# Kernel tuning notes

Hardware: AMD Instinct MI355X
Metric: run time of the kernel (lower is better)

The kernel has to match this reference:

```python
import jax, jax.numpy as jnp
import numpy as np

B, T = 192, 50
VOCAB = 24000
EMBED = 300
HID2 = 2000          # 2*HIDDEN_SIZE
MAXOUT = 300         # DIMEN_MAXOUT_UNIT
QV = 300             # DIMEN_QUALITY_VECTOR
H2 = 100             # LSTM hidden


def setup_inputs():
    key = jax.random.key(0)
    ks = jax.random.split(key, 24)
    s = 0.02
    inp = {
        'dec_out': jax.random.normal(ks[0], (B, T, HID2), jnp.float32),
        'y': jax.random.randint(ks[1], (B, T), 0, VOCAB, jnp.int64 if jax.config.jax_enable_x64 else jnp.int32),
        'contex': jax.random.normal(ks[2], (B, T, HID2), jnp.float32),
        'embed_table': jax.random.normal(ks[3], (VOCAB, EMBED), jnp.float32) * s,
        'W1': jax.random.uniform(ks[4], (VOCAB, QV), jnp.float32),  # torch.rand
        'S_w': jax.random.normal(ks[5], (2 * MAXOUT, HID2), jnp.float32) * s,
        'S_b': jnp.zeros((2 * MAXOUT,), jnp.float32),
        'V_w': jax.random.normal(ks[6], (2 * MAXOUT, 2 * EMBED), jnp.float32) * s,
        'V_b': jnp.zeros((2 * MAXOUT,), jnp.float32),
        'C0_w': jax.random.normal(ks[7], (2 * MAXOUT, HID2), jnp.float32) * s,
        'C0_b': jnp.zeros((2 * MAXOUT,), jnp.float32),
        'W2_w': jax.random.normal(ks[8], (QV, MAXOUT), jnp.float32) * s,
        'W2_b': jnp.zeros((QV,), jnp.float32),
        'wih0': jax.random.normal(ks[9], (4 * H2, QV), jnp.float32) * s,
        'whh0': jax.random.normal(ks[10], (4 * H2, H2), jnp.float32) * s,
        'bih0': jnp.zeros((4 * H2,), jnp.float32),
        'bhh0': jnp.zeros((4 * H2,), jnp.float32),
        'wih1': jax.random.normal(ks[11], (4 * H2, H2), jnp.float32) * s,
        'whh1': jax.random.normal(ks[12], (4 * H2, H2), jnp.float32) * s,
        'bih1': jnp.zeros((4 * H2,), jnp.float32),
        'bhh1': jnp.zeros((4 * H2,), jnp.float32),
        'Wqe_w': jax.random.normal(ks[13], (1, H2), jnp.float32) * s,
        'Wqe_b': jnp.zeros((1,), jnp.float32),
    }
    return inp


def _lstm_layer(x, Wih, Whh, bih, bhh):
    # x: [B, T, D] -> outputs [B, T, H]; torch gate order i, f, g, o
    Bb = x.shape[0]
    H = Whh.shape[1]
    xT = jnp.swapaxes(x, 0, 1)  # [T, B, D]

    def step(carry, xt):
        h, c = carry
        g = xt @ Wih.T + h @ Whh.T + bih + bhh
        i, f, gg, o = jnp.split(g, 4, axis=-1)
        i = jax.nn.sigmoid(i); f = jax.nn.sigmoid(f)
        gg = jnp.tanh(gg); o = jax.nn.sigmoid(o)
        c = f * c + i * gg
        h = o * jnp.tanh(c)
        return (h, c), h

    h0 = jnp.zeros((Bb, H), x.dtype)
    (_, _), hs = jax.lax.scan(step, (h0, h0), xT)
    return jnp.swapaxes(hs, 0, 1)


def reference(dec_out, y, contex, embed_table, W1, S_w, S_b, V_w, V_b,
              C0_w, C0_b, W2_w, W2_b, wih0, whh0, bih0, bhh0,
              wih1, whh1, bih1, bhh1, Wqe_w, Wqe_b):
    Bb, Tt, _ = dec_out.shape
    embed = embed_table[y]  # [B, T, EMBED]
    idx = jnp.arange(Tt)
    li = jnp.where(idx == 0, 1, idx - 1)          # left neighbor (i==0 -> 1)
    ri = jnp.where(idx == Tt - 1, Tt - 2, idx + 1)  # right neighbor (i==T-1 -> T-2)
    tensor2 = jnp.concatenate([embed[:, li], embed[:, ri]], axis=-1)  # [B,T,600]
    t_long = (dec_out @ S_w.T + S_b) + (tensor2 @ V_w.T + V_b) + (contex @ C0_w.T + C0_b)
    # maxout over consecutive pairs: t[...,i] = max(t_long[...,2i], t_long[...,2i+1])
    t = t_long.reshape(Bb, Tt, MAXOUT, 2).max(axis=-1)
    a = t @ W2_w.T + W2_b                        # [B,T,QV]
    logits = a @ W1.T                            # [B,T,VOCAB]
    b = jax.nn.log_softmax(logits.reshape(Bb * Tt, -1), axis=1)
    quality = W1[y] * a                          # [B,T,QV]
    mask = (y == 0)
    index1 = jnp.where(mask.any(axis=1), mask.argmax(axis=1), Tt - 1)
    h = _lstm_layer(quality, wih0, whh0, bih0, bhh0)
    h = _lstm_layer(h, wih1, whh1, bih1, bhh1)   # [B,T,H2]
    s_sel = h[jnp.arange(Bb), index1]            # [B,H2]
    QE_score = jax.nn.sigmoid(s_sel @ Wqe_w.T + Wqe_b)  # [B,1]
    return (b, QE_score)
```

## Files before the change

kernel.cpp:

```cpp
#include <hip/hip_runtime.h>

typedef unsigned short u16;
typedef __attribute__((ext_vector_type(4))) float f32x4;
typedef __attribute__((ext_vector_type(8))) short bf16x8;
typedef __attribute__((ext_vector_type(4))) unsigned short u16x4;
typedef __attribute__((ext_vector_type(8))) unsigned short u16x8;

#define BT 9600
#define VOCAB 24000
#define NCB 188

__device__ __forceinline__ u16 f2b(float f){
  union { float f; unsigned u; } c; c.f = f;
  unsigned u = c.u;
  return (u16)((u + 0x7FFFu + ((u >> 16) & 1u)) >> 16);
}
__device__ __forceinline__ float b2f(u16 v){
  union { unsigned u; float f; } c; c.u = ((unsigned)v) << 16;
  return c.f;
}

#define GLD16(g, l) __builtin_amdgcn_global_load_lds( \
    (__attribute__((address_space(1))) void*)(g), \
    (__attribute__((address_space(3))) void*)(l), 16, 0, 0)

__device__ __forceinline__ void gemm_core(
    const u16* __restrict__ A, const u16* __restrict__ B,
    int K, int brow, int bcol, u16* As, u16* Bs, f32x4 acc[4][4])
{
  const int tid  = threadIdx.x;
  const int w    = tid >> 6;
  const int lane = tid & 63;
  const int wm = w >> 1, wn = w & 1;

  const f32x4 fz = {0.f, 0.f, 0.f, 0.f};
  #pragma unroll
  for (int m = 0; m < 4; ++m)
    #pragma unroll
    for (int n = 0; n < 4; ++n) acc[m][n] = fz;

  const int nkt = K >> 6;

  auto stage = [&](int kt, int buf) {
    #pragma unroll
    for (int i = 0; i < 4; ++i) {
      int gl  = i * 256 + tid;
      int row = gl >> 3;
      int g   = (gl & 7) ^ (row & 7);
      const u16* ga = A + (size_t)(brow + row) * K + (kt << 6) + (g << 3);
      GLD16(ga, As + buf * 8192 + (size_t)(i * 256 + w * 64) * 8);
      const u16* gb = B + (size_t)(bcol + row) * K + (kt << 6) + (g << 3);
      GLD16(gb, Bs + buf * 8192 + (size_t)(i * 256 + w * 64) * 8);
    }
  };

  stage(0, 0);
  int cur = 0;
  for (int kt = 0; kt < nkt; ++kt) {
    if (kt + 1 < nkt) {
      stage(kt + 1, cur ^ 1);
      asm volatile("s_waitcnt vmcnt(8)" ::: "memory");
    } else {
      asm volatile("s_waitcnt vmcnt(0)" ::: "memory");
    }
    __builtin_amdgcn_s_barrier();
    asm volatile("" ::: "memory");
    const u16* Ab = As + cur * 8192;
    const u16* Bb = Bs + cur * 8192;
    #pragma unroll
    for (int kk = 0; kk < 2; ++kk) {
      bf16x8 af[4], bf[4];
      #pragma unroll
      for (int m = 0; m < 4; ++m) {
        int row = wm * 64 + m * 16 + (lane & 15);
        int g   = (kk * 4 + (lane >> 4)) ^ (row & 7);
        af[m] = *(const bf16x8*)(Ab + row * 64 + g * 8);
      }
      #pragma unroll
      for (int n = 0; n < 4; ++n) {
        int row = wn * 64 + n * 16 + (lane & 15);
        int g   = (kk * 4 + (lane >> 4)) ^ (row & 7);
        bf[n] = *(const bf16x8*)(Bb + row * 64 + g * 8);
      }
      #pragma unroll
      for (int m = 0; m < 4; ++m)
        #pragma unroll
        for (int n = 0; n < 4; ++n)
          acc[m][n] = __builtin_amdgcn_mfma_f32_16x16x32_bf16(af[m], bf[n], acc[m][n], 0, 0, 0);
    }
    asm volatile("" ::: "memory");
    __builtin_amdgcn_s_barrier();
    cur ^= 1;
  }
}

__global__ __launch_bounds__(256) void k_prep_main(
    const float* __restrict__ dec, const float* __restrict__ ctx, u16* __restrict__ Xcat)
{
  int tid = blockIdx.x * 256 + threadIdx.x;
  if (tid >= 9600 * 500) return;
  int r = tid / 500, k8 = (tid % 500) * 8;
  const float* src = (k8 < 2000) ? dec + (size_t)r * 2000 + k8
                                 : ctx + (size_t)r * 2000 + (k8 - 2000);
  const float4* s4 = (const float4*)src;
  float4 v0 = s4[0], v1 = s4[1];
  u16x8 o;
  o[0] = f2b(v0.x); o[1] = f2b(v0.y); o[2] = f2b(v0.z); o[3] = f2b(v0.w);
  o[4] = f2b(v1.x); o[5] = f2b(v1.y); o[6] = f2b(v1.z); o[7] = f2b(v1.w);
  *(u16x8*)(Xcat + (size_t)r * 4608 + k8) = o;
}

__global__ __launch_bounds__(256) void k_prep_emb(
    const int* __restrict__ y, const float* __restrict__ etab, u16* __restrict__ Xcat)
{
  int tid = blockIdx.x * 256 + threadIdx.x;
  if (tid >= 9600 * 152) return;
  int r = tid / 152, u = tid % 152;
  u16* xr = Xcat + (size_t)r * 4608;
  if (u >= 150) {
    int base = (u == 150) ? 4300 : 4604;
    u16x4 z; z[0] = 0; z[1] = 0; z[2] = 0; z[3] = 0;
    *(u16x4*)(xr + base) = z;
    return;
  }
  int t = r % 50;
  int side = u / 75, j4 = (u % 75) * 4;
  int tt = (side == 0) ? (t == 0 ? 1 : t - 1) : (t == 49 ? 48 : t + 1);
  int tok = y[r - t + tt];
  float4 v = *(const float4*)(etab + (size_t)tok * 300 + j4);
  u16x4 o; o[0] = f2b(v.x); o[1] = f2b(v.y); o[2] = f2b(v.z); o[3] = f2b(v.w);
  *(u16x4*)(xr + (side == 0 ? 4000 : 4304) + j4) = o;
}

__global__ __launch_bounds__(256) void k_wcat(
    const float* __restrict__ Sw, const float* __restrict__ C0w, const float* __restrict__ Vw,
    const float* __restrict__ Sb, const float* __restrict__ Vb, const float* __restrict__ C0b,
    u16* __restrict__ Wcat, float* __restrict__ biasc)
{
  int tid = blockIdx.x * 256 + threadIdx.x;
  if (tid >= 640 * 4608) return;
  int n = tid / 4608, k = tid % 4608;
  float v = 0.f;
  if (n < 600) {
    if (k < 2000)                  v = Sw[n * 2000 + k];
    else if (k < 4000)             v = C0w[n * 2000 + (k - 2000)];
    else if (k < 4300)             v = Vw[n * 600 + (k - 4000)];
    else if (k >= 4304 && k < 4604) v = Vw[n * 600 + 300 + (k - 4304)];
  }
  Wcat[tid] = f2b(v);
  if (k == 0) biasc[n] = (n < 600) ? (Sb[n] + Vb[n] + C0b[n]) : 0.f;
}

__device__ __forceinline__ void conv_body(
    const float* __restrict__ src, u16* __restrict__ dst,
    int srows, int scols, int drows, int dcols4, int tid)
{
  if (tid >= drows * dcols4) return;
  int r = tid / dcols4, c4 = (tid % dcols4) * 4;
  u16x4 o; o[0] = 0; o[1] = 0; o[2] = 0; o[3] = 0;
  if (r < srows && c4 < scols) {
    float4 v = *(const float4*)(src + (size_t)r * scols + c4);
    o[0] = f2b(v.x); o[1] = f2b(v.y); o[2] = f2b(v.z); o[3] = f2b(v.w);
  }
  *(u16x4*)(dst + (size_t)r * (dcols4 * 4) + c4) = o;
}

__global__ __launch_bounds__(256) void k_conv(
    const float* __restrict__ src, u16* __restrict__ dst,
    int srows, int scols, int drows, int dcols4)
{
  conv_body(src, dst, srows, scols, drows, dcols4, blockIdx.x * 256 + threadIdx.x);
}

__global__ __launch_bounds__(256) void k_conv3(
    const float* __restrict__ W2w, const float* __restrict__ wih0,
    const float* __restrict__ wih1, u16* __restrict__ W2b,
    u16* __restrict__ wih0b, u16* __restrict__ wih1b)
{
  int bid = blockIdx.x;
  if (bid < 120)       conv_body(W2w,  W2b,   300, 300, 384, 80, bid * 256 + threadIdx.x);
  else if (bid < 280)  conv_body(wih0, wih0b, 400, 300, 512, 80, (bid - 120) * 256 + threadIdx.x);
  else                 conv_body(wih1, wih1b, 400, 100, 512, 32, (bid - 280) * 256 + threadIdx.x);
}

__global__ __launch_bounds__(256) void k_gemm_tlong(
    const u16* __restrict__ Xcat, const u16* __restrict__ Wcat,
    const float* __restrict__ biasc, u16* __restrict__ tb)
{
  __shared__ u16 As[16384], Bs[16384];
  f32x4 acc[4][4];
  int brow = blockIdx.y * 128, bcol = blockIdx.x * 128;
  gemm_core(Xcat, Wcat, 4608, brow, bcol, As, Bs, acc);
  int lane = threadIdx.x & 63, w = threadIdx.x >> 6;
  int wm = w >> 1, wn = w & 1;
  #pragma unroll
  for (int m = 0; m < 4; ++m)
    #pragma unroll
    for (int n = 0; n < 4; ++n)
      #pragma unroll
      for (int r = 0; r < 4; ++r) {
        int row = brow + wm * 64 + m * 16 + ((lane >> 4) << 2) + r;
        int col = bcol + wn * 64 + n * 16 + (lane & 15);
        float v = acc[m][n][r] + biasc[col];
        float o = __shfl_xor(v, 1);
        float t = fmaxf(v, o);
        if ((lane & 1) == 0)
          tb[(size_t)row * 320 + (col >> 1)] = f2b(t);
      }
}

__global__ __launch_bounds__(256) void k_gemm_a(
    const u16* __restrict__ tb, const u16* __restrict__ W2b,
    const float* __restrict__ W2bias, const float* __restrict__ W1,
    const int* __restrict__ y, u16* __restrict__ ab, u16* __restrict__ qb)
{
  __shared__ u16 As[16384], Bs[16384];
  f32x4 acc[4][4];
  int brow = blockIdx.y * 128, bcol = blockIdx.x * 128;
  gemm_core(tb, W2b, 320, brow, bcol, As, Bs, acc);
  int lane = threadIdx.x & 63, w = threadIdx.x >> 6;
  int wm = w >> 1, wn = w & 1;
  #pragma unroll
  for (int m = 0; m < 4; ++m)
    #pragma unroll
    for (int n = 0; n < 4; ++n)
      #pragma unroll
      for (int r = 0; r < 4; ++r) {
        int row = brow + wm * 64 + m * 16 + ((lane >> 4) << 2) + r;
        int col = bcol + wn * 64 + n * 16 + (lane & 15);
        if (col < 320) {
          float bias = (col < 300) ? W2bias[col] : 0.f;
          float a = acc[m][n][r] + bias;
          ab[(size_t)row * 320 + col] = f2b(a);
          float q = 0.f;
          if (col < 300) {
            int yv = y[row];
            q = a * W1[(size_t)yv * 300 + col];
          }
          qb[(size_t)row * 320 + col] = f2b(q);
        }
      }
}

template<int BF16OUT>
__global__ __launch_bounds__(256) void k_gemm_logits(
    const u16* __restrict__ ab, const u16* __restrict__ W1b,
    float* __restrict__ dout, u16* __restrict__ lb, float* __restrict__ part)
{
  __shared__ u16 As[16384], Bs[16384];
  __shared__ float rowsum[128][2];
  f32x4 acc[4][4];
  int brow = blockIdx.y * 128, bcol = blockIdx.x * 128;
  gemm_core(ab, W1b, 320, brow, bcol, As, Bs, acc);
  int lane = threadIdx.x & 63, w = threadIdx.x >> 6;
  int wm = w >> 1, wn = w & 1;
  rowsum[threadIdx.x >> 1][threadIdx.x & 1] = 0.f;
  __syncthreads();
  #pragma unroll
  for (int m = 0; m < 4; ++m)
    #pragma unroll
    for (int r = 0; r < 4; ++r) {
      int lrow = wm * 64 + m * 16 + ((lane >> 4) << 2) + r;
      size_t grow = (size_t)(brow + lrow);
      float es = 0.f;
      #pragma unroll
      for (int n = 0; n < 4; ++n) {
        int col = bcol + wn * 64 + n * 16 + (lane & 15);
        float v = acc[m][n][r];
        if (col < VOCAB) {
          if (BF16OUT) lb[grow * 24064 + col] = f2b(v);
          else         dout[grow * VOCAB + col] = v;
          es += __expf(v);
        }
      }
      es += __shfl_xor(es, 1); es += __shfl_xor(es, 2);
      es += __shfl_xor(es, 4); es += __shfl_xor(es, 8);
      if ((lane & 15) == 0) rowsum[lrow][wn] = es;
    }
  __syncthreads();
  if (threadIdx.x < 128)
    part[(size_t)(brow + threadIdx.x) * NCB + blockIdx.x] =
        rowsum[threadIdx.x][0] + rowsum[threadIdx.x][1];
}

__global__ __launch_bounds__(256) void k_gemm_proj(
    const u16* __restrict__ Ab, const u16* __restrict__ Bb, int K,
    const float* __restrict__ b1, const float* __restrict__ b2, float* __restrict__ out)
{
  __shared__ u16 As[16384], Bs[16384];
  f32x4 acc[4][4];
  int brow = blockIdx.y * 128, bcol = blockIdx.x * 128;
  gemm_core(Ab, Bb, K, brow, bcol, As, Bs, acc);
  int lane = threadIdx.x & 63, w = threadIdx.x >> 6;
  int wm = w >> 1, wn = w & 1;
  #pragma unroll
  for (int m = 0; m < 4; ++m)
    #pragma unroll
    for (int n = 0; n < 4; ++n)
      #pragma unroll
      for (int r = 0; r < 4; ++r) {
        int row = brow + wm * 64 + m * 16 + ((lane >> 4) << 2) + r;
        int col = bcol + wn * 64 + n * 16 + (lane & 15);
        if (col < 400)
          out[(size_t)row * 400 + col] = acc[m][n][r] + b1[col] + b2[col];
      }
}

__global__ __launch_bounds__(256) void k_rowlog(
    const float* __restrict__ part, float* __restrict__ logl)
{
  int row = blockIdx.x * 4 + (threadIdx.x >> 6);
  int l = threadIdx.x & 63;
  const float* p = part + (size_t)row * NCB;
  float s = p[l] + p[l + 64] + (l < 60 ? p[l + 128] : 0.f);
  s += __shfl_xor(s, 1);  s += __shfl_xor(s, 2);  s += __shfl_xor(s, 4);
  s += __shfl_xor(s, 8);  s += __shfl_xor(s, 16); s += __shfl_xor(s, 32);
  if (l == 0) logl[row] = logf(s);
}

__global__ __launch_bounds__(256) void k_fixup(
    float4* __restrict__ out4, const float* __restrict__ logl)
{
  size_t i = (size_t)blockIdx.x * blockDim.x + threadIdx.x;
  size_t stride = (size_t)gridDim.x * blockDim.x;
  const size_t total = (size_t)BT * (VOCAB / 4);
  for (; i < total; i += stride) {
    size_t row = i / (VOCAB / 4);
    float l = logl[row];
    float4 v = out4[i];
    v.x -= l; v.y -= l; v.z -= l; v.w -= l;
    out4[i] = v;
  }
}

__global__ __launch_bounds__(256) void k_fixup_bf16(
    const u16* __restrict__ lb, const float* __restrict__ logl, float* __restrict__ out)
{
  size_t i = (size_t)blockIdx.x * blockDim.x + threadIdx.x;
  size_t stride = (size_t)gridDim.x * blockDim.x;
  const size_t total = (size_t)BT * (VOCAB / 8);
  for (; i < total; i += stride) {
    size_t row = i / (VOCAB / 8);
    int c8 = (int)(i % (VOCAB / 8)) * 8;
    float l = logl[row];
    u16x8 v = *(const u16x8*)(lb + row * 24064 + c8);
    float4 o0, o1;
    o0.x = b2f(v[0]) - l; o0.y = b2f(v[1]) - l; o0.z = b2f(v[2]) - l; o0.w = b2f(v[3]) - l;
    o1.x = b2f(v[4]) - l; o1.y = b2f(v[5]) - l; o1.z = b2f(v[6]) - l; o1.w = b2f(v[7]) - l;
    float* op = out + row * VOCAB + c8;
    *(float4*)op = o0;
    *(float4*)(op + 4) = o1;
  }
}

__global__ __launch_bounds__(512) void k_lstm0(
    const float* __restrict__ xp0, const float* __restrict__ whh0, u16* __restrict__ h0b)
{
  int b = blockIdx.x, g = threadIdx.x;
  __shared__ float h[100];
  __shared__ float act[400];
  float wrow[100];
  if (g < 400) {
    const float4* wr = (const float4*)(whh0 + (size_t)g * 100);
    #pragma unroll
    for (int q = 0; q < 25; ++q) {
      float4 t = wr[q];
      wrow[4 * q] = t.x; wrow[4 * q + 1] = t.y; wrow[4 * q + 2] = t.z; wrow[4 * q + 3] = t.w;
    }
  }
  if (g < 100) h[g] = 0.f;
  float c = 0.f;
  __syncthreads();
  for (int t = 0; t < 50; ++t) {
    if (g < 400) {
      float s = xp0[(size_t)(b * 50 + t) * 400 + g];
      const float4* hv = (const float4*)h;
      #pragma unroll
      for (int q = 0; q < 25; ++q) {
        float4 hh = hv[q];
        s += wrow[4 * q] * hh.x + wrow[4 * q + 1] * hh.y
           + wrow[4 * q + 2] * hh.z + wrow[4 * q + 3] * hh.w;
      }
      act[g] = (g >= 200 && g < 300) ? tanhf(s) : 1.f / (1.f + __expf(-s));
    }
    __syncthreads();
    if (g < 100) {
      c = act[100 + g] * c + act[g] * act[200 + g];
      float hn = act[300 + g] * tanhf(c);
      h[g] = hn;
      h0b[(size_t)(b * 50 + t) * 128 + g] = f2b(hn);
    } else if (g < 128) {
      h0b[(size_t)(b * 50 + t) * 128 + g] = 0;
    }
    __syncthreads();
  }
}

__global__ __launch_bounds__(512) void k_lstm1(
    const float* __restrict__ xp1, const float* __restrict__ whh1,
    const int* __restrict__ y, const float* __restrict__ wqe,
    const float* __restrict__ wqeb, float* __restrict__ qout)
{
  int b = blockIdx.x, g = threadIdx.x;
  __shared__ float h[100];
  __shared__ float act[400];
  __shared__ float hsel[100];
  __shared__ int idx1;
  float wrow[100];
  if (g < 400) {
    const float4* wr = (const float4*)(whh1 + (size_t)g * 100);
    #pragma unroll
    for (int q = 0; q < 25; ++q) {
      float4 t = wr[q];
      wrow[4 * q] = t.x; wrow[4 * q + 1] = t.y; wrow[4 * q + 2] = t.z; wrow[4 * q + 3] = t.w;
    }
  }
  if (g == 0) {
    int ix = 49;
    for (int t = 0; t < 50; ++t) { if (y[b * 50 + t] == 0) { ix = t; break; } }
    idx1 = ix;
  }
  if (g < 100) { h[g] = 0.f; hsel[g] = 0.f; }
  float c = 0.f;
  __syncthreads();
  for (int t = 0; t < 50; ++t) {
    if (g < 400) {
      float s = xp1[(size_t)(b * 50 + t) * 400 + g];
      const float4* hv = (const float4*)h;
      #pragma unroll
      for (int q = 0; q < 25; ++q) {
        float4 hh = hv[q];
        s += wrow[4 * q] * hh.x + wrow[4 * q + 1] * hh.y
           + wrow[4 * q + 2] * hh.z + wrow[4 * q + 3] * hh.w;
      }
      act[g] = (g >= 200 && g < 300) ? tanhf(s) : 1.f / (1.f + __expf(-s));
    }
    __syncthreads();
    if (g < 100) {
      c = act[100 + g] * c + act[g] * act[200 + g];
      float hn = act[300 + g] * tanhf(c);
      h[g] = hn;
      if (t == idx1) hsel[g] = hn;
    }
    __syncthreads();
  }
  if (g == 0) {
    float s = wqeb[0];
    for (int j = 0; j < 100; ++j) s += hsel[j] * wqe[j];
    qout[b] = 1.f / (1.f + __expf(-s));
  }
}

extern "C" void kernel_launch(void* const* d_in, const int* in_sizes, int n_in,
                              void* d_out, int out_size, void* d_ws, size_t ws_size,
                              hipStream_t stream) {
  const float* dec  = (const float*)d_in[0];
  const int*   y    = (const int*)d_in[1];
  const float* ctx  = (const float*)d_in[2];
  const float* etab = (const float*)d_in[3];
  const float* W1   = (const float*)d_in[4];
  const float* Sw   = (const float*)d_in[5];
  const float* Sb   = (const float*)d_in[6];
  const float* Vw   = (const float*)d_in[7];
  const float* Vb   = (const float*)d_in[8];
  const float* C0w  = (const float*)d_in[9];
  const float* C0b  = (const float*)d_in[10];
  const float* W2w  = (const float*)d_in[11];
  const float* W2bias = (const float*)d_in[12];
  const float* wih0 = (const float*)d_in[13];
  const float* whh0 = (const float*)d_in[14];
  const float* bih0 = (const float*)d_in[15];
  const float* bhh0 = (const float*)d_in[16];
  const float* wih1 = (const float*)d_in[17];
  const float* whh1 = (const float*)d_in[18];
  const float* bih1 = (const float*)d_in[19];
  const float* bhh1 = (const float*)d_in[20];
  const float* wqe  = (const float*)d_in[21];
  const float* wqeb = (const float*)d_in[22];

  char* ws = (char*)d_ws;
  u16*   Xcat  = (u16*)(ws + 0);
  u16*   Wcat  = (u16*)(ws + 88473600);
  float* biasc = (float*)(ws + 94371840);
  u16*   tb    = (u16*)(ws + 94374400);
  u16*   W2b   = (u16*)(ws + 100518400);
  u16*   ab    = (u16*)(ws + 100764160);
  u16*   qb    = (u16*)(ws + 106908160);
  u16*   W1b   = (u16*)(ws + 113052160);
  float* part  = (float*)(ws + 128453120);
  float* logl  = (float*)(ws + 135672320);
  u16*   wih0b = (u16*)(ws + 135710720);
  float* xp0   = (float*)(ws + 136038400);
  u16*   h0b   = (u16*)(ws + 151398400);
  u16*   wih1b = (u16*)(ws + 153856000);
  float* xp1   = (float*)(ws + 153987072);
  u16*   lb    = (u16*)(ws + 169347072);
  const size_t WS_NEED_BF16 = 169347072ull + 462028800ull;
  const bool use_bf16_logits = (ws_size >= WS_NEED_BF16);

  float* bout  = (float*)d_out;
  float* qeout = bout + (size_t)BT * VOCAB;

  k_prep_main<<<18750, 256, 0, stream>>>(dec, ctx, Xcat);
  k_prep_emb<<<5700, 256, 0, stream>>>(y, etab, Xcat);
  k_wcat<<<11520, 256, 0, stream>>>(Sw, C0w, Vw, Sb, Vb, C0b, Wcat, biasc);
  k_conv<<<7520, 256, 0, stream>>>(W1, W1b, 24000, 300, 24064, 80);
  k_conv3<<<344, 256, 0, stream>>>(W2w, wih0, wih1, W2b, wih0b, wih1b);
  k_conv<<<64, 256, 0, stream>>>(wih1, wih1b, 400, 100, 512, 32);

  k_gemm_tlong<<<dim3(5, 75), 256, 0, stream>>>(Xcat, Wcat, biasc, tb);
  k_gemm_a<<<dim3(3, 75), 256, 0, stream>>>(tb, W2b, W2bias, W1, y, ab, qb);
  if (use_bf16_logits) {
    k_gemm_logits<1><<<dim3(NCB, 75), 256, 0, stream>>>(ab, W1b, bout, lb, part);
    k_rowlog<<<2400, 256, 0, stream>>>(part, logl);
    k_fixup_bf16<<<4096, 256, 0, stream>>>(lb, logl, bout);
  } else {
    k_gemm_logits<0><<<dim3(NCB, 75), 256, 0, stream>>>(ab, W1b, bout, lb, part);
    k_rowlog<<<2400, 256, 0, stream>>>(part, logl);
    k_fixup<<<4096, 256, 0, stream>>>((float4*)bout, logl);
  }

  k_gemm_proj<<<dim3(4, 75), 256, 0, stream>>>(qb, wih0b, 320, bih0, bhh0, xp0);
  k_lstm0<<<192, 512, 0, stream>>>(xp0, whh0, h0b);
  k_gemm_proj<<<dim3(4, 75), 256, 0, stream>>>(h0b, wih1b, 128, bih1, bhh1, xp1);
  k_lstm1<<<192, 512, 0, stream>>>(xp1, whh1, y, wqe, wqeb, qeout);
}
```

Measured before the change: 1.036 ms.

## Fuse prep kernels, chunk bf16 logits into L2-resident row blocks, stage stores

Merges all the input and weight conversion kernels into one launch. Splits the bf16 logits path into three row chunks so the bf16 logits buffer is a third the size and may stay in the last-level cache between the GEMM and the fixup pass. The GEMM epilogue now stages the tile in shared memory and writes coalesced 16-byte rows. This adds launches and exposes some serialization between chunks, and the smaller workspace requirement changes when the bf16 path is chosen.

Result: no change. 1.048 ms (+1.1%).

```diff
diff --git a/kernel.cpp b/kernel.cpp
--- a/kernel.cpp
+++ b/kernel.cpp
@@ -94,10 +94,10 @@
   }
 }
 
-__global__ __launch_bounds__(256) void k_prep_main(
-    const float* __restrict__ dec, const float* __restrict__ ctx, u16* __restrict__ Xcat)
-{
-  int tid = blockIdx.x * 256 + threadIdx.x;
+__device__ __forceinline__ void prep_main_body(
+    const float* __restrict__ dec, const float* __restrict__ ctx,
+    u16* __restrict__ Xcat, int tid)
+{
   if (tid >= 9600 * 500) return;
   int r = tid / 500, k8 = (tid % 500) * 8;
   const float* src = (k8 < 2000) ? dec + (size_t)r * 2000 + k8
@@ -110,10 +110,10 @@
   *(u16x8*)(Xcat + (size_t)r * 4608 + k8) = o;
 }
 
-__global__ __launch_bounds__(256) void k_prep_emb(
-    const int* __restrict__ y, const float* __restrict__ etab, u16* __restrict__ Xcat)
-{
-  int tid = blockIdx.x * 256 + threadIdx.x;
+__device__ __forceinline__ void prep_emb_body(
+    const int* __restrict__ y, const float* __restrict__ etab,
+    u16* __restrict__ Xcat, int tid)
+{
   if (tid >= 9600 * 152) return;
   int r = tid / 152, u = tid % 152;
   u16* xr = Xcat + (size_t)r * 4608;
@@ -132,12 +132,11 @@
   *(u16x4*)(xr + (side == 0 ? 4000 : 4304) + j4) = o;
 }
 
-__global__ __launch_bounds__(256) void k_wcat(
+__device__ __forceinline__ void wcat_body(
     const float* __restrict__ Sw, const float* __restrict__ C0w, const float* __restrict__ Vw,
     const float* __restrict__ Sb, const float* __restrict__ Vb, const float* __restrict__ C0b,
-    u16* __restrict__ Wcat, float* __restrict__ biasc)
-{
-  int tid = blockIdx.x * 256 + threadIdx.x;
+    u16* __restrict__ Wcat, float* __restrict__ biasc, int tid)
+{
   if (tid >= 640 * 4608) return;
   int n = tid / 4608, k = tid % 4608;
   float v = 0.f;
@@ -165,22 +164,26 @@
   *(u16x4*)(dst + (size_t)r * (dcols4 * 4) + c4) = o;
 }
 
-__global__ __launch_bounds__(256) void k_conv(
-    const float* __restrict__ src, u16* __restrict__ dst,
-    int srows, int scols, int drows, int dcols4)
-{
-  conv_body(src, dst, srows, scols, drows, dcols4, blockIdx.x * 256 + threadIdx.x);
-}
-
-__global__ __launch_bounds__(256) void k_conv3(
-    const float* __restrict__ W2w, const float* __restrict__ wih0,
-    const float* __restrict__ wih1, u16* __restrict__ W2b,
+__global__ __launch_bounds__(256) void k_prep_all(
+    const float* __restrict__ dec, const float* __restrict__ ctx,
+    const int* __restrict__ y, const float* __restrict__ etab,
+    const float* __restrict__ Sw, const float* __restrict__ C0w,
+    const float* __restrict__ Vw, const float* __restrict__ Sb,
+    const float* __restrict__ Vb, const float* __restrict__ C0b,
+    const float* __restrict__ W1, const float* __restrict__ W2w,
+    const float* __restrict__ wih0, const float* __restrict__ wih1,
+    u16* __restrict__ Xcat, u16* __restrict__ Wcat, float* __restrict__ biasc,
+    u16* __restrict__ W1b, u16* __restrict__ W2b,
     u16* __restrict__ wih0b, u16* __restrict__ wih1b)
 {
-  int bid = blockIdx.x;
-  if (bid < 120)       conv_body(W2w,  W2b,   300, 300, 384, 80, bid * 256 + threadIdx.x);
-  else if (bid < 280)  conv_body(wih0, wih0b, 400, 300, 512, 80, (bid - 120) * 256 + threadIdx.x);
-  else                 conv_body(wih1, wih1b, 400, 100, 512, 32, (bid - 280) * 256 + threadIdx.x);
+  int bid = blockIdx.x, th = threadIdx.x;
+  if (bid < 18750)      prep_main_body(dec, ctx, Xcat, bid * 256 + th);
+  else if (bid < 24450) prep_emb_body(y, etab, Xcat, (bid - 18750) * 256 + th);
+  else if (bid < 35970) wcat_body(Sw, C0w, Vw, Sb, Vb, C0b, Wcat, biasc, (bid - 24450) * 256 + th);
+  else if (bid < 43490) conv_body(W1,   W1b,   24000, 300, 24064, 80, (bid - 35970) * 256 + th);
+  else if (bid < 43610) conv_body(W2w,  W2b,   300,   300, 384,   80, (bid - 43490) * 256 + th);
+  else if (bid < 43770) conv_body(wih0, wih0b, 400,   300, 512,   80, (bid - 43610) * 256 + th);
+  else                  conv_body(wih1, wih1b, 400,   100, 512,   32, (bid - 43770) * 256 + th);
 }
 
 __global__ __launch_bounds__(256) void k_gemm_tlong(
@@ -242,10 +245,52 @@
       }
 }
 
-template<int BF16OUT>
-__global__ __launch_bounds__(256) void k_gemm_logits(
+__global__ __launch_bounds__(256) void k_gemm_logits_bf16(
     const u16* __restrict__ ab, const u16* __restrict__ W1b,
-    float* __restrict__ dout, u16* __restrict__ lb, float* __restrict__ part)
+    u16* __restrict__ lb, float* __restrict__ part, int rb0)
+{
+  __shared__ u16 smem[32768];
+  __shared__ float rowsum[128][2];
+  f32x4 acc[4][4];
+  int brow = (rb0 + blockIdx.y) * 128, bcol = blockIdx.x * 128;
+  gemm_core(ab, W1b, 320, brow, bcol, smem, smem + 16384, acc);
+  int lane = threadIdx.x & 63, w = threadIdx.x >> 6;
+  int wm = w >> 1, wn = w & 1;
+  #pragma unroll
+  for (int m = 0; m < 4; ++m)
+    #pragma unroll
+    for (int r = 0; r < 4; ++r) {
+      int lrow = wm * 64 + m * 16 + ((lane >> 4) << 2) + r;
+      float es = 0.f;
+      #pragma unroll
+      for (int n = 0; n < 4; ++n) {
+        int lcol = wn * 64 + n * 16 + (lane & 15);
+        float v = acc[m][n][r];
+        smem[lrow * 136 + lcol] = f2b(v);
+        if (bcol + lcol < VOCAB) es += __expf(v);
+      }
+      es += __shfl_xor(es, 1); es += __shfl_xor(es, 2);
+      es += __shfl_xor(es, 4); es += __shfl_xor(es, 8);
+      if ((lane & 15) == 0) rowsum[lrow][wn] = es;
+    }
+  __syncthreads();
+  if (threadIdx.x < 128)
+    part[(size_t)(brow + threadIdx.x) * NCB + blockIdx.x] =
+        rowsum[threadIdx.x][0] + rowsum[threadIdx.x][1];
+  int lrow_base = blockIdx.y * 128;
+  #pragma unroll
+  for (int j = 0; j < 8; ++j) {
+    int ch   = j * 256 + threadIdx.x;
+    int rowl = ch >> 4;
+    int c16  = (ch & 15) << 3;
+    u16x8 v = *(const u16x8*)(smem + rowl * 136 + c16);
+    *(u16x8*)(lb + (size_t)(lrow_base + rowl) * 24064 + bcol + c16) = v;
+  }
+}
+
+__global__ __launch_bounds__(256) void k_gemm_logits_f32(
+    const u16* __restrict__ ab, const u16* __restrict__ W1b,
+    float* __restrict__ dout, float* __restrict__ part)
 {
   __shared__ u16 As[16384], Bs[16384];
   __shared__ float rowsum[128][2];
@@ -254,8 +299,6 @@
   gemm_core(ab, W1b, 320, brow, bcol, As, Bs, acc);
   int lane = threadIdx.x & 63, w = threadIdx.x >> 6;
   int wm = w >> 1, wn = w & 1;
-  rowsum[threadIdx.x >> 1][threadIdx.x & 1] = 0.f;
-  __syncthreads();
   #pragma unroll
   for (int m = 0; m < 4; ++m)
     #pragma unroll
@@ -268,8 +311,7 @@
         int col = bcol + wn * 64 + n * 16 + (lane & 15);
         float v = acc[m][n][r];
         if (col < VOCAB) {
-          if (BF16OUT) lb[grow * 24064 + col] = f2b(v);
-          else         dout[grow * VOCAB + col] = v;
+          dout[grow * VOCAB + col] = v;
           es += __expf(v);
         }
       }
@@ -307,9 +349,9 @@
 }
 
 __global__ __launch_bounds__(256) void k_rowlog(
-    const float* __restrict__ part, float* __restrict__ logl)
-{
-  int row = blockIdx.x * 4 + (threadIdx.x >> 6);
+    const float* __restrict__ part, float* __restrict__ logl, int r0)
+{
+  int row = r0 + blockIdx.x * 4 + (threadIdx.x >> 6);
   int l = threadIdx.x & 63;
   const float* p = part + (size_t)row * NCB;
   float s = p[l] + p[l + 64] + (l < 60 ? p[l + 128] : 0.f);
@@ -334,16 +376,18 @@
 }
 
 __global__ __launch_bounds__(256) void k_fixup_bf16(
-    const u16* __restrict__ lb, const float* __restrict__ logl, float* __restrict__ out)
+    const u16* __restrict__ lb, const float* __restrict__ logl,
+    float* __restrict__ out, int r0, int nrows)
 {
   size_t i = (size_t)blockIdx.x * blockDim.x + threadIdx.x;
   size_t stride = (size_t)gridDim.x * blockDim.x;
-  const size_t total = (size_t)BT * (VOCAB / 8);
+  const size_t total = (size_t)nrows * (VOCAB / 8);
   for (; i < total; i += stride) {
-    size_t row = i / (VOCAB / 8);
+    size_t rowl = i / (VOCAB / 8);
     int c8 = (int)(i % (VOCAB / 8)) * 8;
+    size_t row = r0 + rowl;
     float l = logl[row];
-    u16x8 v = *(const u16x8*)(lb + row * 24064 + c8);
+    u16x8 v = *(const u16x8*)(lb + rowl * 24064 + c8);
     float4 o0, o1;
     o0.x = b2f(v[0]) - l; o0.y = b2f(v[1]) - l; o0.z = b2f(v[2]) - l; o0.w = b2f(v[3]) - l;
     o1.x = b2f(v[4]) - l; o1.y = b2f(v[5]) - l; o1.z = b2f(v[6]) - l; o1.w = b2f(v[7]) - l;
@@ -495,28 +539,28 @@
   u16*   wih1b = (u16*)(ws + 153856000);
   float* xp1   = (float*)(ws + 153987072);
   u16*   lb    = (u16*)(ws + 169347072);
-  const size_t WS_NEED_BF16 = 169347072ull + 462028800ull;
+  const size_t WS_NEED_BF16 = 169347072ull + 154009600ull;
   const bool use_bf16_logits = (ws_size >= WS_NEED_BF16);
 
   float* bout  = (float*)d_out;
   float* qeout = bout + (size_t)BT * VOCAB;
 
-  k_prep_main<<<18750, 256, 0, stream>>>(dec, ctx, Xcat);
-  k_prep_emb<<<5700, 256, 0, stream>>>(y, etab, Xcat);
-  k_wcat<<<11520, 256, 0, stream>>>(Sw, C0w, Vw, Sb, Vb, C0b, Wcat, biasc);
-  k_conv<<<7520, 256, 0, stream>>>(W1, W1b, 24000, 300, 24064, 80);
-  k_conv3<<<344, 256, 0, stream>>>(W2w, wih0, wih1, W2b, wih0b, wih1b);
-  k_conv<<<64, 256, 0, stream>>>(wih1, wih1b, 400, 100, 512, 32);
+  k_prep_all<<<43834, 256, 0, stream>>>(dec, ctx, y, etab, Sw, C0w, Vw, Sb, Vb, C0b,
+                                        W1, W2w, wih0, wih1,
+                                        Xcat, Wcat, biasc, W1b, W2b, wih0b, wih1b);
 
   k_gemm_tlong<<<dim3(5, 75), 256, 0, stream>>>(Xcat, Wcat, biasc, tb);
   k_gemm_a<<<dim3(3, 75), 256, 0, stream>>>(tb, W2b, W2bias, W1, y, ab, qb);
+
   if (use_bf16_logits) {
-    k_gemm_logits<1><<<dim3(NCB, 75), 256, 0, stream>>>(ab, W1b, bout, lb, part);
-    k_rowlog<<<2400, 256, 0, stream>>>(part, logl);
-    k_fixup_bf16<<<4096, 256, 0, stream>>>(lb, logl, bout);
+    for (int c = 0; c < 3; ++c) {
+      k_gemm_logits_bf16<<<dim3(NCB, 25), 256, 0, stream>>>(ab, W1b, lb, part, 25 * c);
+      k_rowlog<<<800, 256, 0, stream>>>(part, logl, 3200 * c);
+      k_fixup_bf16<<<2048, 256, 0, stream>>>(lb, logl, bout, 3200 * c, 3200);
+    }
   } else {
-    k_gemm_logits<0><<<dim3(NCB, 75), 256, 0, stream>>>(ab, W1b, bout, lb, part);
-    k_rowlog<<<2400, 256, 0, stream>>>(part, logl);
+    k_gemm_logits_f32<<<dim3(NCB, 75), 256, 0, stream>>>(ab, W1b, bout, part);
+    k_rowlog<<<2400, 256, 0, stream>>>(part, logl, 0);
     k_fixup<<<4096, 256, 0, stream>>>((float4*)bout, logl);
   }
 
```
